# Optimization experiments

Hardware: AMD Instinct MI355X
Metric: run time of the kernel (lower is better)

## Reference

```python
import jax, jax.numpy as jnp
import numpy as np

N_NODES = 50000
N_EDGES = 600000
IN_DIM = 128
HID = 128


def setup_inputs() -> dict:
    key = jax.random.key(0)
    ks = jax.random.split(key, 8)
    x = jax.random.normal(ks[0], (N_NODES, IN_DIM), dtype=jnp.float32)
    edge_index = jax.random.randint(ks[1], (2, N_EDGES), 0, N_NODES, dtype=jnp.int64)
    def lin(k, fan_in, fan_out):
        s = 1.0 / np.sqrt(fan_in)
        kw, kb = jax.random.split(k)
        W = jax.random.uniform(kw, (fan_in, fan_out), jnp.float32, -s, s)
        b = jax.random.uniform(kb, (fan_out,), jnp.float32, -s, s)
        return W, b
    W0, b0 = lin(ks[2], IN_DIM, HID)
    W1, b1 = lin(ks[3], HID, HID)
    W2, b2 = lin(ks[4], HID, HID)
    return {"x": x, "edge_index": edge_index, "W0": W0, "b0": b0,
            "W1": W1, "b1": b1, "W2": W2, "b2": b2}


def reference(x, edge_index, W0, b0, W1, b1, W2, b2):
    n = x.shape[0]
    loops = jnp.arange(n, dtype=edge_index.dtype)
    src = jnp.concatenate([edge_index[0], loops])  # source nodes (+self loops)
    dst = jnp.concatenate([edge_index[1], loops])  # destination nodes
    # symmetric GCN normalization: deg^{-1/2}[src] * deg^{-1/2}[dst]
    deg = jax.ops.segment_sum(jnp.ones(src.shape[0], x.dtype), dst, num_segments=n)
    dinv = jnp.where(deg > 0, jax.lax.rsqrt(deg), 0.0)
    norm = dinv[src] * dinv[dst]  # [E+N]

    def gcn_layer(h, W, b):
        hw = h @ W                              # [N, H]
        msg = hw[src] * norm[:, None]           # gather + scale, [E+N, H]
        agg = jax.ops.segment_sum(msg, dst, num_segments=n)  # scatter-add
        return agg + b

    h = x
    for W, b in ((W0, b0), (W1, b1), (W2, b2)):
        h = jax.nn.relu(gcn_layer(h, W, b))     # dropout is identity in eval
    return h  # JK='last'
```

## Files before the change

### kernel.cpp

```cpp
#include <hip/hip_runtime.h>

#define NN 50000
#define NE 600000
#define DIM 128
#define NB_N 196
#define NB_E 2344
#define TILES 3125
#define ROWW 136
#define NEPAD (NE + 8 * NN + 64)

typedef unsigned short u16;
typedef unsigned int u32;
typedef __attribute__((ext_vector_type(8))) short bf16x8;
typedef __attribute__((ext_vector_type(4))) float f32x4;

__device__ __forceinline__ u16 f2bf(float f) {
    u32 u = __builtin_bit_cast(u32, f);
    u32 r = (u + 0x7FFFu + ((u >> 16) & 1u)) >> 16;
    return (u16)r;
}
__device__ __forceinline__ float bflo(u32 w) { return __builtin_bit_cast(float, w << 16); }
__device__ __forceinline__ float bfhi(u32 w) { return __builtin_bit_cast(float, w & 0xffff0000u); }
__device__ __forceinline__ float i2f(int b) { return __builtin_bit_cast(float, b); }


__global__ __launch_bounds__(256) void k_count(const int* __restrict__ ei,
                                               int* __restrict__ deg) {
    __shared__ int s64;
    if (threadIdx.x == 0) {
        int o = 0;
#pragma unroll
        for (int j = 0; j < 16; j++) o |= ei[2 * j + 1];
        s64 = (o == 0);
    }
    __syncthreads();
    int e = blockIdx.x * 256 + threadIdx.x;
    if (e >= NE) return;
    int d = s64 ? ei[2 * (NE + e)] : ei[NE + e];
    atomicAdd(&deg[d], 1);
}

__global__ __launch_bounds__(256) void k_scanA(const int* __restrict__ deg,
                                               int* __restrict__ rp8,
                                               int* __restrict__ bsum) {
    __shared__ int buf[256];
    int t = threadIdx.x, i = blockIdx.x * 256 + t;
    int v = 0;
    if (i < NN) {
        v = (deg[i] + 7) & ~7;
        if (v == 0) v = 8;
    }
    buf[t] = v;
    __syncthreads();
    for (int off = 1; off < 256; off <<= 1) {
        int x = (t >= off) ? buf[t - off] : 0;
        __syncthreads();
        buf[t] += x;
        __syncthreads();
    }
    if (i < NN) rp8[i] = buf[t] - v;
    if (t == 255) bsum[blockIdx.x] = buf[255];
}

__global__ __launch_bounds__(256) void k_scanB(int* __restrict__ bsum) {
    __shared__ int buf[256];
    int t = threadIdx.x;
    int v = (t < NB_N) ? bsum[t] : 0;
    buf[t] = v;
    __syncthreads();
    for (int off = 1; off < 256; off <<= 1) {
        int x = (t >= off) ? buf[t - off] : 0;
        __syncthreads();
        buf[t] += x;
        __syncthreads();
    }
    bsum[t] = buf[t] - v;
}

__global__ __launch_bounds__(256) void k_scanC(const int* __restrict__ deg,
                                               int* __restrict__ rp8,
                                               const int* __restrict__ bsum,
                                               float* __restrict__ dinv) {
    int i = blockIdx.x * 256 + threadIdx.x;
    if (i < NN) {
        rp8[i] += bsum[i >> 8];
        dinv[i] = rsqrtf((float)(deg[i] + 1));
    }
    if (i == 0) rp8[NN] = bsum[255];
}

__global__ __launch_bounds__(256) void k_fill(const int* __restrict__ ei,
                                              const int* __restrict__ rp8,
                                              int* __restrict__ cursor,
                                              const float* __restrict__ dinv,
                                              int2* __restrict__ recs) {
    __shared__ int s64;
    if (threadIdx.x == 0) {
        int o = 0;
#pragma unroll
        for (int j = 0; j < 16; j++) o |= ei[2 * j + 1];
        s64 = (o == 0);
    }
    __syncthreads();
    int e = blockIdx.x * 256 + threadIdx.x;
    if (e >= NE) return;
    int is64 = s64;
    int s = is64 ? ei[2 * e] : ei[e];
    int d = is64 ? ei[2 * (NE + e)] : ei[NE + e];
    int pos = rp8[d] + atomicAdd(&cursor[d], 1);
    int2 rc;
    rc.x = s;
    rc.y = __builtin_bit_cast(int, dinv[s] * dinv[d]);
    recs[pos] = rc;
}

__global__ __launch_bounds__(256) void k_wcast(const float* __restrict__ W0,
                                               const float* __restrict__ W1,
                                               const float* __restrict__ W2,
                                               u16* __restrict__ Wt) {
    int idx = blockIdx.x * 256 + threadIdx.x;
    int l = idx >> 14, rem = idx & 16383;
    int n = rem >> 7, k = rem & 127;
    const float* W = (l == 0) ? W0 : ((l == 1) ? W1 : W2);
    Wt[idx] = f2bf(W[k * 128 + n]);
}

__global__ __launch_bounds__(256) void k_gemm_f32(const float* __restrict__ x,
                                                  const u16* __restrict__ Wt,
                                                  u16* __restrict__ hwb) {
    int lane = threadIdx.x & 63;
    int tile = blockIdx.x * 4 + (threadIdx.x >> 6);
    if (tile >= TILES) return;
    int r = lane & 15, q = lane >> 4;

    bf16x8 Bf[8][4];
#pragma unroll
    for (int nt = 0; nt < 8; nt++)
#pragma unroll
        for (int kc = 0; kc < 4; kc++)
            Bf[nt][kc] = *(const bf16x8*)(Wt + ((nt * 16 + r) << 7) + kc * 32 + q * 8);

    long rowbase = (long)tile * 16;
    bf16x8 Af[4];
#pragma unroll
    for (int kc = 0; kc < 4; kc++) {
        const float4* p = (const float4*)(x + (rowbase + r) * 128 + kc * 32 + q * 8);
        float4 t0 = p[0], t1 = p[1];
        bf16x8 a;
        a[0] = (short)f2bf(t0.x); a[1] = (short)f2bf(t0.y);
        a[2] = (short)f2bf(t0.z); a[3] = (short)f2bf(t0.w);
        a[4] = (short)f2bf(t1.x); a[5] = (short)f2bf(t1.y);
        a[6] = (short)f2bf(t1.z); a[7] = (short)f2bf(t1.w);
        Af[kc] = a;
    }

#pragma unroll
    for (int nt = 0; nt < 8; nt++) {
        f32x4 acc = {0.f, 0.f, 0.f, 0.f};
#pragma unroll
        for (int kc = 0; kc < 4; kc++)
            acc = __builtin_amdgcn_mfma_f32_16x16x32_bf16(Af[kc], Bf[nt][kc], acc, 0, 0, 0);
#pragma unroll
        for (int i = 0; i < 4; i++)
            hwb[(rowbase + q * 4 + i) * 128 + nt * 16 + r] = f2bf(acc[i]);
    }
}

__device__ __forceinline__ void fma8(float* acc, uint4 u, float n) {
    acc[0] += n * bflo(u.x); acc[1] += n * bfhi(u.x);
    acc[2] += n * bflo(u.y); acc[3] += n * bfhi(u.y);
    acc[4] += n * bflo(u.z); acc[5] += n * bfhi(u.z);
    acc[6] += n * bflo(u.w); acc[7] += n * bfhi(u.w);
}

__device__ __forceinline__ void self_init(const u16* hw, float dv, int v, int g,
                                          int r, float* acc) {
    uint4 sv = *(const uint4*)(hw + (size_t)v * DIM + r * 8);
    float sc = (g == 0) ? dv * dv : 0.0f;
    acc[0] = sc * bflo(sv.x); acc[1] = sc * bfhi(sv.x);
    acc[2] = sc * bflo(sv.y); acc[3] = sc * bfhi(sv.y);
    acc[4] = sc * bflo(sv.z); acc[5] = sc * bfhi(sv.z);
    acc[6] = sc * bflo(sv.w); acc[7] = sc * bfhi(sv.w);
}

__device__ __forceinline__ void combine_bias_relu(const float* bias, int r,
                                                  float* acc) {
#pragma unroll
    for (int j = 0; j < 8; j++) {
        acc[j] += __shfl_xor(acc[j], 16, 64);
        acc[j] += __shfl_xor(acc[j], 32, 64);
    }
    float4 b0 = ((const float4*)bias)[2 * r];
    float4 b1 = ((const float4*)bias)[2 * r + 1];
    acc[0] = fmaxf(acc[0] + b0.x, 0.f); acc[1] = fmaxf(acc[1] + b0.y, 0.f);
    acc[2] = fmaxf(acc[2] + b0.z, 0.f); acc[3] = fmaxf(acc[3] + b0.w, 0.f);
    acc[4] = fmaxf(acc[4] + b1.x, 0.f); acc[5] = fmaxf(acc[5] + b1.y, 0.f);
    acc[6] = fmaxf(acc[6] + b1.z, 0.f); acc[7] = fmaxf(acc[7] + b1.w, 0.f);
}

__device__ __forceinline__ void agg_pair(const u16* __restrict__ hw,
                                         const int* __restrict__ rp8,
                                         const int2* __restrict__ recs,
                                         const float* __restrict__ dinv,
                                         int va, int vb, int g, int r,
                                         float* A, float* B) {
    self_init(hw, dinv[va], va, g, r, A);
    self_init(hw, dinv[vb], vb, g, r, B);
    int ea = rp8[va], enda = rp8[va + 1];
    int eb = rp8[vb], endb = rp8[vb + 1];
    int4 qa = *(const int4*)(recs + ea + 2 * g);
    int4 qb = *(const int4*)(recs + eb + 2 * g);
    while (ea < enda || eb < endb) {
        float na0 = (ea < enda) ? i2f(qa.y) : 0.f;
        float na1 = (ea < enda) ? i2f(qa.w) : 0.f;
        float nb0 = (eb < endb) ? i2f(qb.y) : 0.f;
        float nb1 = (eb < endb) ? i2f(qb.w) : 0.f;
        uint4 ua0 = *(const uint4*)(hw + (size_t)(u32)qa.x * DIM + r * 8);
        uint4 ua1 = *(const uint4*)(hw + (size_t)(u32)qa.z * DIM + r * 8);
        uint4 ub0 = *(const uint4*)(hw + (size_t)(u32)qb.x * DIM + r * 8);
        uint4 ub1 = *(const uint4*)(hw + (size_t)(u32)qb.z * DIM + r * 8);
        ea += 8; eb += 8;
        int pa = min(ea, enda - 8);
        int pb = min(eb, endb - 8);
        int4 qa_n = *(const int4*)(recs + pa + 2 * g);
        int4 qb_n = *(const int4*)(recs + pb + 2 * g);
        fma8(A, ua0, na0); fma8(A, ua1, na1);
        fma8(B, ub0, nb0); fma8(B, ub1, nb1);
        qa = qa_n; qb = qb_n;
    }
}

__global__ __launch_bounds__(256) void k_agg_gemm(const u16* __restrict__ hw_in,
                                                  const int* __restrict__ rp8,
                                                  const int2* __restrict__ recs,
                                                  const float* __restrict__ dinv,
                                                  const float* __restrict__ bias,
                                                  const u16* __restrict__ Wt,
                                                  u16* __restrict__ hw_out) {
    __shared__ u16 sm[16 * ROWW];
    int lane = threadIdx.x & 63;
    int w = threadIdx.x >> 6;
    int g = lane >> 4, r = lane & 15;
    int base = blockIdx.x * 16;
#pragma unroll
    for (int p = 0; p < 2; p++) {
        int rowa = w * 4 + 2 * p;
        int va = base + rowa;
        float A[8], B[8];
        agg_pair(hw_in, rp8, recs, dinv, va, va + 1, g, r, A, B);
        combine_bias_relu(bias, r, A);
        combine_bias_relu(bias, r, B);
        if (g == 0) {
            uint4 pk;
            pk.x = (u32)f2bf(A[0]) | ((u32)f2bf(A[1]) << 16);
            pk.y = (u32)f2bf(A[2]) | ((u32)f2bf(A[3]) << 16);
            pk.z = (u32)f2bf(A[4]) | ((u32)f2bf(A[5]) << 16);
            pk.w = (u32)f2bf(A[6]) | ((u32)f2bf(A[7]) << 16);
            *(uint4*)(sm + rowa * ROWW + r * 8) = pk;
            pk.x = (u32)f2bf(B[0]) | ((u32)f2bf(B[1]) << 16);
            pk.y = (u32)f2bf(B[2]) | ((u32)f2bf(B[3]) << 16);
            pk.z = (u32)f2bf(B[4]) | ((u32)f2bf(B[5]) << 16);
            pk.w = (u32)f2bf(B[6]) | ((u32)f2bf(B[7]) << 16);
            *(uint4*)(sm + (rowa + 1) * ROWW + r * 8) = pk;
        }
    }
    __syncthreads();
    int q = lane >> 4;
    bf16x8 Af[4];
#pragma unroll
    for (int kc = 0; kc < 4; kc++)
        Af[kc] = *(const bf16x8*)(sm + r * ROWW + kc * 32 + q * 8);
#pragma unroll
    for (int t = 0; t < 2; t++) {
        int nt = w * 2 + t;
        f32x4 acc = {0.f, 0.f, 0.f, 0.f};
#pragma unroll
        for (int kc = 0; kc < 4; kc++) {
            bf16x8 Bf = *(const bf16x8*)(Wt + ((nt * 16 + r) << 7) + kc * 32 + q * 8);
            acc = __builtin_amdgcn_mfma_f32_16x16x32_bf16(Af[kc], Bf, acc, 0, 0, 0);
        }
#pragma unroll
        for (int i = 0; i < 4; i++)
            hw_out[(size_t)(base + q * 4 + i) * DIM + nt * 16 + r] = f2bf(acc[i]);
    }
}

__global__ __launch_bounds__(256) void k_agg_out(const u16* __restrict__ hw_in,
                                                 const int* __restrict__ rp8,
                                                 const int2* __restrict__ recs,
                                                 const float* __restrict__ dinv,
                                                 const float* __restrict__ bias,
                                                 float* __restrict__ out) {
    int lane = threadIdx.x & 63;
    int w = threadIdx.x >> 6;
    int g = lane >> 4, r = lane & 15;
    int va = blockIdx.x * 8 + w * 2;
    float A[8], B[8];
    agg_pair(hw_in, rp8, recs, dinv, va, va + 1, g, r, A, B);
    combine_bias_relu(bias, r, A);
    combine_bias_relu(bias, r, B);
    if (g == 0) {
        float4* p = (float4*)(out + (size_t)va * DIM + r * 8);
        p[0] = make_float4(A[0], A[1], A[2], A[3]);
        p[1] = make_float4(A[4], A[5], A[6], A[7]);
        p = (float4*)(out + (size_t)(va + 1) * DIM + r * 8);
        p[0] = make_float4(B[0], B[1], B[2], B[3]);
        p[1] = make_float4(B[4], B[5], B[6], B[7]);
    }
}


extern "C" void kernel_launch(void* const* d_in, const int* in_sizes, int n_in,
                              void* d_out, int out_size, void* d_ws, size_t ws_size,
                              hipStream_t stream) {
    const float* x = (const float*)d_in[0];
    const int* ei = (const int*)d_in[1];
    const float* W0 = (const float*)d_in[2];
    const float* b0 = (const float*)d_in[3];
    const float* W1 = (const float*)d_in[4];
    const float* b1 = (const float*)d_in[5];
    const float* W2 = (const float*)d_in[6];
    const float* b2 = (const float*)d_in[7];

    char* ws = (char*)d_ws;
    size_t off = 0;
    auto alloc = [&](size_t bytes) -> void* {
        void* p = ws + off;
        off += (bytes + 511) & ~(size_t)511;
        return p;
    };
    int* deg = (int*)alloc(NN * 4);
    int* cursor = (int*)alloc(NN * 4);
    int2* recs = (int2*)alloc((size_t)NEPAD * 8);
    size_t zbytes = off;
    float* dinv = (float*)alloc(NN * 4);
    int* rp8 = (int*)alloc((NN + 1) * 4);
    int* bsum = (int*)alloc(256 * 4);
    u16* Wt = (u16*)alloc(3 * 128 * 128 * 2);
    u16* hwA = (u16*)alloc((size_t)NN * DIM * 2);
    u16* hwB = (u16*)alloc((size_t)NN * DIM * 2);

    hipMemsetAsync(ws, 0, zbytes, stream);
    k_count<<<NB_E, 256, 0, stream>>>(ei, deg);
    k_scanA<<<NB_N, 256, 0, stream>>>(deg, rp8, bsum);
    k_scanB<<<1, 256, 0, stream>>>(bsum);
    k_scanC<<<NB_N, 256, 0, stream>>>(deg, rp8, bsum, dinv);
    k_fill<<<NB_E, 256, 0, stream>>>(ei, rp8, cursor, dinv, recs);
    k_wcast<<<192, 256, 0, stream>>>(W0, W1, W2, Wt);

    k_gemm_f32<<<(TILES + 3) / 4, 256, 0, stream>>>(x, Wt, hwA);
    k_agg_gemm<<<TILES, 256, 0, stream>>>(hwA, rp8, recs, dinv, b0,
                                          Wt + 16384, hwB);
    k_agg_gemm<<<TILES, 256, 0, stream>>>(hwB, rp8, recs, dinv, b1,
                                          Wt + 32768, hwA);
    k_agg_out<<<NN / 8, 256, 0, stream>>>(hwA, rp8, recs, dinv, b2,
                                          (float*)d_out);
}
```

Measured before the change: 277.9 us.

## Factor GCN normalization into pre/post row scaling and shrink edge records

The edge weight dinv[s]*dinv[d] is split into a source-side scale applied when each GEMM writes its output rows and a destination-side scale applied after aggregation. This lets each edge record shrink from (src, norm) int2 to a single int, halving index traffic and turning the inner loop into plain adds. Padding slots now point at a zeroed dummy row NN instead of carrying a zero weight, and the padding fill is done in the fill kernel. The three scan kernels are merged into one single-block scan, and the weight cast is folded into the fill kernel to cut launches. Rounding the dinv-scaled values to bf16 before aggregation slightly changes numerics, and the serial single-block scan may be slow.

Result: slower. 375.2 us (+35.0%).

```diff
diff --git a/kernel.cpp b/kernel.cpp
--- a/kernel.cpp
+++ b/kernel.cpp
@@ -21,7 +21,10 @@
 }
 __device__ __forceinline__ float bflo(u32 w) { return __builtin_bit_cast(float, w << 16); }
 __device__ __forceinline__ float bfhi(u32 w) { return __builtin_bit_cast(float, w & 0xffff0000u); }
-__device__ __forceinline__ float i2f(int b) { return __builtin_bit_cast(float, b); }
+__device__ __forceinline__ int pad8(int d) {
+    int p = (d + 7) & ~7;
+    return p < 8 ? 8 : p;
+}
 
 
 __global__ __launch_bounds__(256) void k_count(const int* __restrict__ ei,
@@ -40,60 +43,43 @@
     atomicAdd(&deg[d], 1);
 }
 
-__global__ __launch_bounds__(256) void k_scanA(const int* __restrict__ deg,
+__global__ __launch_bounds__(1024) void k_scan(const int* __restrict__ deg,
                                                int* __restrict__ rp8,
-                                               int* __restrict__ bsum) {
-    __shared__ int buf[256];
-    int t = threadIdx.x, i = blockIdx.x * 256 + t;
-    int v = 0;
-    if (i < NN) {
-        v = (deg[i] + 7) & ~7;
-        if (v == 0) v = 8;
-    }
-    buf[t] = v;
+                                               float* __restrict__ dinv) {
+    __shared__ int buf[1024];
+    int t = threadIdx.x;
+    int start = t * 49, end = min(start + 49, NN);
+    int s = 0;
+    for (int i = start; i < end; i++) s += pad8(deg[i]);
+    buf[t] = s;
     __syncthreads();
-    for (int off = 1; off < 256; off <<= 1) {
+    for (int off = 1; off < 1024; off <<= 1) {
         int x = (t >= off) ? buf[t - off] : 0;
         __syncthreads();
         buf[t] += x;
         __syncthreads();
     }
-    if (i < NN) rp8[i] = buf[t] - v;
-    if (t == 255) bsum[blockIdx.x] = buf[255];
-}
-
-__global__ __launch_bounds__(256) void k_scanB(int* __restrict__ bsum) {
-    __shared__ int buf[256];
-    int t = threadIdx.x;
-    int v = (t < NB_N) ? bsum[t] : 0;
-    buf[t] = v;
-    __syncthreads();
-    for (int off = 1; off < 256; off <<= 1) {
-        int x = (t >= off) ? buf[t - off] : 0;
-        __syncthreads();
-        buf[t] += x;
-        __syncthreads();
-    }
-    bsum[t] = buf[t] - v;
-}
-
-__global__ __launch_bounds__(256) void k_scanC(const int* __restrict__ deg,
-                                               int* __restrict__ rp8,
-                                               const int* __restrict__ bsum,
-                                               float* __restrict__ dinv) {
-    int i = blockIdx.x * 256 + threadIdx.x;
-    if (i < NN) {
-        rp8[i] += bsum[i >> 8];
-        dinv[i] = rsqrtf((float)(deg[i] + 1));
-    }
-    if (i == 0) rp8[NN] = bsum[255];
+    int run = buf[t] - s;
+    for (int i = start; i < end; i++) {
+        int d = deg[i];
+        rp8[i] = run;
+        dinv[i] = rsqrtf((float)(d + 1));
+        run += pad8(d);
+    }
+    if (t == 1023) rp8[NN] = buf[1023];
 }
 
 __global__ __launch_bounds__(256) void k_fill(const int* __restrict__ ei,
                                               const int* __restrict__ rp8,
                                               int* __restrict__ cursor,
-                                              const float* __restrict__ dinv,
-                                              int2* __restrict__ recs) {
+                                              const int* __restrict__ deg,
+                                              int* __restrict__ recs,
+                                              const float* __restrict__ W0,
+                                              const float* __restrict__ W1,
+                                              const float* __restrict__ W2,
+                                              u16* __restrict__ Wt,
+                                              u16* __restrict__ hwA,
+                                              u16* __restrict__ hwB) {
     __shared__ int s64;
     if (threadIdx.x == 0) {
         int o = 0;
@@ -103,30 +89,37 @@
     }
     __syncthreads();
     int e = blockIdx.x * 256 + threadIdx.x;
-    if (e >= NE) return;
-    int is64 = s64;
-    int s = is64 ? ei[2 * e] : ei[e];
-    int d = is64 ? ei[2 * (NE + e)] : ei[NE + e];
-    int pos = rp8[d] + atomicAdd(&cursor[d], 1);
-    int2 rc;
-    rc.x = s;
-    rc.y = __builtin_bit_cast(int, dinv[s] * dinv[d]);
-    recs[pos] = rc;
-}
-
-__global__ __launch_bounds__(256) void k_wcast(const float* __restrict__ W0,
-                                               const float* __restrict__ W1,
-                                               const float* __restrict__ W2,
-                                               u16* __restrict__ Wt) {
-    int idx = blockIdx.x * 256 + threadIdx.x;
-    int l = idx >> 14, rem = idx & 16383;
-    int n = rem >> 7, k = rem & 127;
-    const float* W = (l == 0) ? W0 : ((l == 1) ? W1 : W2);
-    Wt[idx] = f2bf(W[k * 128 + n]);
+    if (e < NE) {
+        int is64 = s64;
+        int s = is64 ? ei[2 * e] : ei[e];
+        int d = is64 ? ei[2 * (NE + e)] : ei[NE + e];
+        int pos = rp8[d] + atomicAdd(&cursor[d], 1);
+        recs[pos] = s;
+    }
+    int b = blockIdx.x;
+    if (b < 192) {
+        int idx = b * 256 + threadIdx.x;
+        int l = idx >> 14, rem = idx & 16383;
+        int n = rem >> 7, k = rem & 127;
+        const float* W = (l == 0) ? W0 : ((l == 1) ? W1 : W2);
+        Wt[idx] = f2bf(W[k * 128 + n]);
+    } else if (b < 388) {
+        int i = (b - 192) * 256 + threadIdx.x;
+        if (i < NN) {
+            int rp = rp8[i], d = deg[i], p = pad8(d);
+            for (int j = d; j < p; j++) recs[rp + j] = NN;
+        }
+    } else if (b == 388) {
+        if (threadIdx.x < 64) {
+            ((u32*)(hwA + (size_t)NN * DIM))[threadIdx.x] = 0;
+            ((u32*)(hwB + (size_t)NN * DIM))[threadIdx.x] = 0;
+        }
+    }
 }
 
 __global__ __launch_bounds__(256) void k_gemm_f32(const float* __restrict__ x,
                                                   const u16* __restrict__ Wt,
+                                                  const float* __restrict__ dinv,
                                                   u16* __restrict__ hwb) {
     int lane = threadIdx.x & 63;
     int tile = blockIdx.x * 4 + (threadIdx.x >> 6);
@@ -154,6 +147,10 @@
         Af[kc] = a;
     }
 
+    float dv[4];
+#pragma unroll
+    for (int i = 0; i < 4; i++) dv[i] = dinv[rowbase + q * 4 + i];
+
 #pragma unroll
     for (int nt = 0; nt < 8; nt++) {
         f32x4 acc = {0.f, 0.f, 0.f, 0.f};
@@ -162,29 +159,58 @@
             acc = __builtin_amdgcn_mfma_f32_16x16x32_bf16(Af[kc], Bf[nt][kc], acc, 0, 0, 0);
 #pragma unroll
         for (int i = 0; i < 4; i++)
-            hwb[(rowbase + q * 4 + i) * 128 + nt * 16 + r] = f2bf(acc[i]);
-    }
-}
-
-__device__ __forceinline__ void fma8(float* acc, uint4 u, float n) {
-    acc[0] += n * bflo(u.x); acc[1] += n * bfhi(u.x);
-    acc[2] += n * bflo(u.y); acc[3] += n * bfhi(u.y);
-    acc[4] += n * bflo(u.z); acc[5] += n * bfhi(u.z);
-    acc[6] += n * bflo(u.w); acc[7] += n * bfhi(u.w);
-}
-
-__device__ __forceinline__ void self_init(const u16* hw, float dv, int v, int g,
-                                          int r, float* acc) {
-    uint4 sv = *(const uint4*)(hw + (size_t)v * DIM + r * 8);
-    float sc = (g == 0) ? dv * dv : 0.0f;
-    acc[0] = sc * bflo(sv.x); acc[1] = sc * bfhi(sv.x);
-    acc[2] = sc * bflo(sv.y); acc[3] = sc * bfhi(sv.y);
-    acc[4] = sc * bflo(sv.z); acc[5] = sc * bfhi(sv.z);
-    acc[6] = sc * bflo(sv.w); acc[7] = sc * bfhi(sv.w);
-}
-
-__device__ __forceinline__ void combine_bias_relu(const float* bias, int r,
-                                                  float* acc) {
+            hwb[(rowbase + q * 4 + i) * 128 + nt * 16 + r] = f2bf(dv[i] * acc[i]);
+    }
+}
+
+__device__ __forceinline__ void add8(float* a, uint4 u) {
+    a[0] += bflo(u.x); a[1] += bfhi(u.x);
+    a[2] += bflo(u.y); a[3] += bfhi(u.y);
+    a[4] += bflo(u.z); a[5] += bfhi(u.z);
+    a[6] += bflo(u.w); a[7] += bfhi(u.w);
+}
+
+__device__ __forceinline__ void agg_pair(const u16* __restrict__ hw,
+                                         const int* __restrict__ rp8,
+                                         const int* __restrict__ recs,
+                                         int va, int vb, int g, int r,
+                                         float* A, float* B) {
+    uint4 sva = *(const uint4*)(hw + (size_t)va * DIM + r * 8);
+    uint4 svb = *(const uint4*)(hw + (size_t)vb * DIM + r * 8);
+    float m = (g == 0) ? 1.0f : 0.0f;
+    A[0] = m * bflo(sva.x); A[1] = m * bfhi(sva.x);
+    A[2] = m * bflo(sva.y); A[3] = m * bfhi(sva.y);
+    A[4] = m * bflo(sva.z); A[5] = m * bfhi(sva.z);
+    A[6] = m * bflo(sva.w); A[7] = m * bfhi(sva.w);
+    B[0] = m * bflo(svb.x); B[1] = m * bfhi(svb.x);
+    B[2] = m * bflo(svb.y); B[3] = m * bfhi(svb.y);
+    B[4] = m * bflo(svb.z); B[5] = m * bfhi(svb.z);
+    B[6] = m * bflo(svb.w); B[7] = m * bfhi(svb.w);
+
+    int ea = rp8[va], enda = rp8[va + 1];
+    int eb = rp8[vb], endb = rp8[vb + 1];
+    int2 qa = *(const int2*)(recs + ea + 2 * g);
+    int2 qb = *(const int2*)(recs + eb + 2 * g);
+    while (ea < enda || eb < endb) {
+        int sa0 = (ea < enda) ? qa.x : NN;
+        int sa1 = (ea < enda) ? qa.y : NN;
+        int sb0 = (eb < endb) ? qb.x : NN;
+        int sb1 = (eb < endb) ? qb.y : NN;
+        uint4 ua0 = *(const uint4*)(hw + (size_t)(u32)sa0 * DIM + r * 8);
+        uint4 ua1 = *(const uint4*)(hw + (size_t)(u32)sa1 * DIM + r * 8);
+        uint4 ub0 = *(const uint4*)(hw + (size_t)(u32)sb0 * DIM + r * 8);
+        uint4 ub1 = *(const uint4*)(hw + (size_t)(u32)sb1 * DIM + r * 8);
+        ea += 8; eb += 8;
+        int2 qa_n = *(const int2*)(recs + min(ea, enda - 8) + 2 * g);
+        int2 qb_n = *(const int2*)(recs + min(eb, endb - 8) + 2 * g);
+        add8(A, ua0); add8(A, ua1);
+        add8(B, ub0); add8(B, ub1);
+        qa = qa_n; qb = qb_n;
+    }
+}
+
+__device__ __forceinline__ void combine_scale(float dv, const float* bias, int r,
+                                              float* acc) {
 #pragma unroll
     for (int j = 0; j < 8; j++) {
         acc[j] += __shfl_xor(acc[j], 16, 64);
@@ -192,47 +218,19 @@
     }
     float4 b0 = ((const float4*)bias)[2 * r];
     float4 b1 = ((const float4*)bias)[2 * r + 1];
-    acc[0] = fmaxf(acc[0] + b0.x, 0.f); acc[1] = fmaxf(acc[1] + b0.y, 0.f);
-    acc[2] = fmaxf(acc[2] + b0.z, 0.f); acc[3] = fmaxf(acc[3] + b0.w, 0.f);
-    acc[4] = fmaxf(acc[4] + b1.x, 0.f); acc[5] = fmaxf(acc[5] + b1.y, 0.f);
-    acc[6] = fmaxf(acc[6] + b1.z, 0.f); acc[7] = fmaxf(acc[7] + b1.w, 0.f);
-}
-
-__device__ __forceinline__ void agg_pair(const u16* __restrict__ hw,
-                                         const int* __restrict__ rp8,
-                                         const int2* __restrict__ recs,
-                                         const float* __restrict__ dinv,
-                                         int va, int vb, int g, int r,
-                                         float* A, float* B) {
-    self_init(hw, dinv[va], va, g, r, A);
-    self_init(hw, dinv[vb], vb, g, r, B);
-    int ea = rp8[va], enda = rp8[va + 1];
-    int eb = rp8[vb], endb = rp8[vb + 1];
-    int4 qa = *(const int4*)(recs + ea + 2 * g);
-    int4 qb = *(const int4*)(recs + eb + 2 * g);
-    while (ea < enda || eb < endb) {
-        float na0 = (ea < enda) ? i2f(qa.y) : 0.f;
-        float na1 = (ea < enda) ? i2f(qa.w) : 0.f;
-        float nb0 = (eb < endb) ? i2f(qb.y) : 0.f;
-        float nb1 = (eb < endb) ? i2f(qb.w) : 0.f;
-        uint4 ua0 = *(const uint4*)(hw + (size_t)(u32)qa.x * DIM + r * 8);
-        uint4 ua1 = *(const uint4*)(hw + (size_t)(u32)qa.z * DIM + r * 8);
-        uint4 ub0 = *(const uint4*)(hw + (size_t)(u32)qb.x * DIM + r * 8);
-        uint4 ub1 = *(const uint4*)(hw + (size_t)(u32)qb.z * DIM + r * 8);
-        ea += 8; eb += 8;
-        int pa = min(ea, enda - 8);
-        int pb = min(eb, endb - 8);
-        int4 qa_n = *(const int4*)(recs + pa + 2 * g);
-        int4 qb_n = *(const int4*)(recs + pb + 2 * g);
-        fma8(A, ua0, na0); fma8(A, ua1, na1);
-        fma8(B, ub0, nb0); fma8(B, ub1, nb1);
-        qa = qa_n; qb = qb_n;
-    }
+    acc[0] = fmaxf(fmaf(dv, acc[0], b0.x), 0.f);
+    acc[1] = fmaxf(fmaf(dv, acc[1], b0.y), 0.f);
+    acc[2] = fmaxf(fmaf(dv, acc[2], b0.z), 0.f);
+    acc[3] = fmaxf(fmaf(dv, acc[3], b0.w), 0.f);
+    acc[4] = fmaxf(fmaf(dv, acc[4], b1.x), 0.f);
+    acc[5] = fmaxf(fmaf(dv, acc[5], b1.y), 0.f);
+    acc[6] = fmaxf(fmaf(dv, acc[6], b1.z), 0.f);
+    acc[7] = fmaxf(fmaf(dv, acc[7], b1.w), 0.f);
 }
 
 __global__ __launch_bounds__(256) void k_agg_gemm(const u16* __restrict__ hw_in,
                                                   const int* __restrict__ rp8,
-                                                  const int2* __restrict__ recs,
+                                                  const int* __restrict__ recs,
                                                   const float* __restrict__ dinv,
                                                   const float* __restrict__ bias,
                                                   const u16* __restrict__ Wt,
@@ -247,9 +245,9 @@
         int rowa = w * 4 + 2 * p;
         int va = base + rowa;
         float A[8], B[8];
-        agg_pair(hw_in, rp8, recs, dinv, va, va + 1, g, r, A, B);
-        combine_bias_relu(bias, r, A);
-        combine_bias_relu(bias, r, B);
+        agg_pair(hw_in, rp8, recs, va, va + 1, g, r, A, B);
+        combine_scale(dinv[va], bias, r, A);
+        combine_scale(dinv[va + 1], bias, r, B);
         if (g == 0) {
             uint4 pk;
             pk.x = (u32)f2bf(A[0]) | ((u32)f2bf(A[1]) << 16);
@@ -270,6 +268,9 @@
 #pragma unroll
     for (int kc = 0; kc < 4; kc++)
         Af[kc] = *(const bf16x8*)(sm + r * ROWW + kc * 32 + q * 8);
+    float dv[4];
+#pragma unroll
+    for (int i = 0; i < 4; i++) dv[i] = dinv[base + q * 4 + i];
 #pragma unroll
     for (int t = 0; t < 2; t++) {
         int nt = w * 2 + t;
@@ -281,13 +282,13 @@
         }
 #pragma unroll
         for (int i = 0; i < 4; i++)
-            hw_out[(size_t)(base + q * 4 + i) * DIM + nt * 16 + r] = f2bf(acc[i]);
+            hw_out[(size_t)(base + q * 4 + i) * DIM + nt * 16 + r] = f2bf(dv[i] * acc[i]);
     }
 }
 
 __global__ __launch_bounds__(256) void k_agg_out(const u16* __restrict__ hw_in,
                                                  const int* __restrict__ rp8,
-                                                 const int2* __restrict__ recs,
+                                                 const int* __restrict__ recs,
                                                  const float* __restrict__ dinv,
                                                  const float* __restrict__ bias,
                                                  float* __restrict__ out) {
@@ -296,9 +297,9 @@
     int g = lane >> 4, r = lane & 15;
     int va = blockIdx.x * 8 + w * 2;
     float A[8], B[8];
-    agg_pair(hw_in, rp8, recs, dinv, va, va + 1, g, r, A, B);
-    combine_bias_relu(bias, r, A);
-    combine_bias_relu(bias, r, B);
+    agg_pair(hw_in, rp8, recs, va, va + 1, g, r, A, B);
+    combine_scale(dinv[va], bias, r, A);
+    combine_scale(dinv[va + 1], bias, r, B);
     if (g == 0) {
         float4* p = (float4*)(out + (size_t)va * DIM + r * 8);
         p[0] = make_float4(A[0], A[1], A[2], A[3]);
@@ -331,28 +332,24 @@
     };
     int* deg = (int*)alloc(NN * 4);
     int* cursor = (int*)alloc(NN * 4);
-    int2* recs = (int2*)alloc((size_t)NEPAD * 8);
     size_t zbytes = off;
+    int* recs = (int*)alloc((size_t)NEPAD * 4);
     float* dinv = (float*)alloc(NN * 4);
     int* rp8 = (int*)alloc((NN + 1) * 4);
-    int* bsum = (int*)alloc(256 * 4);
     u16* Wt = (u16*)alloc(3 * 128 * 128 * 2);
-    u16* hwA = (u16*)alloc((size_t)NN * DIM * 2);
-    u16* hwB = (u16*)alloc((size_t)NN * DIM * 2);
+    u16* hwA = (u16*)alloc((size_t)(NN + 1) * DIM * 2);
+    u16* hwB = (u16*)alloc((size_t)(NN + 1) * DIM * 2);
 
     hipMemsetAsync(ws, 0, zbytes, stream);
     k_count<<<NB_E, 256, 0, stream>>>(ei, deg);
-    k_scanA<<<NB_N, 256, 0, stream>>>(deg, rp8, bsum);
-    k_scanB<<<1, 256, 0, stream>>>(bsum);
-    k_scanC<<<NB_N, 256, 0, stream>>>(deg, rp8, bsum, dinv);
-    k_fill<<<NB_E, 256, 0, stream>>>(ei, rp8, cursor, dinv, recs);
-    k_wcast<<<192, 256, 0, stream>>>(W0, W1, W2, Wt);
-
-    k_gemm_f32<<<(TILES + 3) / 4, 256, 0, stream>>>(x, Wt, hwA);
+    k_scan<<<1, 1024, 0, stream>>>(deg, rp8, dinv);
+    k_fill<<<NB_E, 256, 0, stream>>>(ei, rp8, cursor, deg, recs,
+                                     W0, W1, W2, Wt, hwA, hwB);
+    k_gemm_f32<<<(TILES + 3) / 4, 256, 0, stream>>>(x, Wt, dinv, hwA);
     k_agg_gemm<<<TILES, 256, 0, stream>>>(hwA, rp8, recs, dinv, b0,
                                           Wt + 16384, hwB);
     k_agg_gemm<<<TILES, 256, 0, stream>>>(hwB, rp8, recs, dinv, b1,
                                           Wt + 32768, hwA);
-    k_agg_out<<<NN / 8, 256, 0, stream>>>(hwA, rp8, recs, dinv, b2,
-                                          (float*)d_out);
-}
+    k_agg_out<<<6250, 256, 0, stream>>>(hwA, rp8, recs, dinv, b2,
+                                        (float*)d_out);
+}
```
